# Optimization experiments

Measured on AMD Instinct MI355X. Metric: run time of the kernel, lower is better.

Reference implementation:

```python
import jax, jax.numpy as jnp
import numpy as np

N_NODES = 100000
N_EDGES = 1200000
D = 64
E_CHARGE = np.float32(1.602176634e-19)   # elementary charge (fp32, like the torch buffer)
EPS0 = np.float32(8.8541878128e-12)      # vacuum permittivity (fp32 buffer)


def _mish(x):
    return x * jnp.tanh(jax.nn.softplus(x))


def _mlp(x, w1, b1, w2, b2):
    # nn.Linear convention: y = x @ W.T + b
    h = _mish(x @ w1.T + b1)
    return h @ w2.T + b2


def setup_inputs() -> dict:
    key = jax.random.key(0)
    ks = jax.random.split(key, 20)
    s = 1.0 / np.sqrt(D)
    inp = {
        "node_feats": jax.random.normal(ks[0], (N_NODES, D), jnp.float32),
        "edge_feats": jax.random.normal(ks[1], (N_EDGES, D), jnp.float32),
        "src": jax.random.randint(ks[2], (N_EDGES,), 0, N_NODES),
        "dst": jax.random.randint(ks[3], (N_EDGES,), 0, N_NODES),
    }
    names = ["ws", "wd", "we", "wm"]
    i = 4
    for nm in names:
        inp[nm + "_w1"] = jax.random.normal(ks[i], (D, D), jnp.float32) * s; i += 1
        inp[nm + "_b1"] = jax.random.normal(ks[i], (D,), jnp.float32) * s; i += 1
        inp[nm + "_w2"] = jax.random.normal(ks[i], (D, D), jnp.float32) * s; i += 1
        inp[nm + "_b2"] = jax.random.normal(ks[i], (D,), jnp.float32) * s; i += 1
    return inp


def reference(node_feats, edge_feats, src, dst,
              ws_w1, ws_b1, ws_w2, ws_b2,
              wd_w1, wd_b1, wd_w2, wd_b2,
              we_w1, we_b1, we_w2, we_b2,
              wm_w1, wm_b1, wm_w2, wm_b2):
    # node MLPs then per-edge gather
    h_src = _mlp(node_feats, ws_w1, ws_b1, ws_w2, ws_b2)[src]   # [E, D]
    h_dst = _mlp(node_feats, wd_w1, wd_b1, wd_w2, wd_b2)[dst]   # [E, D]
    ef = _mlp(edge_feats, we_w1, we_b1, we_w2, we_b2)            # [E, D]
    # h_nodes * e^2 / (4*pi*eps0 * edge * 1e-10), all in fp32 like torch
    num = h_src * h_dst * (E_CHARGE ** 2)
    den = np.float32(4.0 * np.pi) * EPS0 * ef * np.float32(1e-10)
    h_nodes = num / den                                          # [E, D]
    m = _mlp(h_nodes, wm_w1, wm_b1, wm_w2, wm_b2)                # [E, D]
    # scatter-sum messages into destination nodes
    h = jax.ops.segment_sum(m, dst, num_segments=N_NODES)        # [N, D]
    return jax.nn.softplus(node_feats + h)
```

## Files before the change

### kernel.cpp

```cpp
#include <hip/hip_runtime.h>
#include <math.h>

#define NNODES 100000
#define NEDGES 1200000
#define TPB_E  5

#define C_EC   1.602176634e-19f
#define C_E2   (C_EC * C_EC)
#define C_4PI  12.566370614359172f
#define C_EPS0 8.8541878128e-12f
#define C_A    (C_4PI * C_EPS0)
#define C_B    1e-10f

typedef __attribute__((ext_vector_type(8))) short bf16x8;
typedef __attribute__((ext_vector_type(4))) float f32x4;
typedef __attribute__((ext_vector_type(4))) unsigned short u16x4;

__device__ __forceinline__ void wave_sync() {
    __builtin_amdgcn_fence(__ATOMIC_ACQ_REL, "wavefront");
    __builtin_amdgcn_wave_barrier();
}

__device__ __forceinline__ unsigned short f2bf(float f) {
    unsigned u = __float_as_uint(f);
    u += 0x7fffu + ((u >> 16) & 1u);
    return (unsigned short)(u >> 16);
}
__device__ __forceinline__ float bf2f(unsigned short s) {
    return __uint_as_float(((unsigned)s) << 16);
}
__device__ __forceinline__ float softplus_f(float x) {
    return fmaxf(x, 0.0f) + log1pf(__expf(-fabsf(x)));
}
__device__ __forceinline__ float mish_f(float x) {
    float e = __expf(fminf(x, 30.0f));
    float n = e * e + 2.0f * e;
    return x * n * __builtin_amdgcn_rcpf(n + 2.0f);
}

__device__ __forceinline__ bf16x8 pack_bf16(float4 a, float4 b) {
    bf16x8 r;
    r[0] = f2bf(a.x); r[1] = f2bf(a.y); r[2] = f2bf(a.z); r[3] = f2bf(a.w);
    r[4] = f2bf(b.x); r[5] = f2bf(b.y); r[6] = f2bf(b.z); r[7] = f2bf(b.w);
    return r;
}


__device__ __forceinline__ void mfma_regs(bf16x8 a0, bf16x8 a1,
                                          const unsigned short* __restrict__ wg,
                                          const float bv[4], int l15, int q,
                                          f32x4 acc[4])
{
    #pragma unroll
    for (int t = 0; t < 4; ++t) {
        acc[t] = (f32x4){bv[t], bv[t], bv[t], bv[t]};
        bf16x8 b0 = *(const bf16x8*)(wg + (t * 16 + l15) * 64 + q * 8);
        bf16x8 b1 = *(const bf16x8*)(wg + (t * 16 + l15) * 64 + 32 + q * 8);
        acc[t] = __builtin_amdgcn_mfma_f32_16x16x32_bf16(a0, b0, acc[t], 0, 0, 0);
        acc[t] = __builtin_amdgcn_mfma_f32_16x16x32_bf16(a1, b1, acc[t], 0, 0, 0);
    }
}

__device__ __forceinline__ void mfma_lds(const unsigned short* hw,
                                         const unsigned short* __restrict__ wg,
                                         const float bv[4], int l15, int q,
                                         f32x4 acc[4])
{
    bf16x8 a0 = *(const bf16x8*)(hw + l15 * 72 + q * 8);
    bf16x8 a1 = *(const bf16x8*)(hw + l15 * 72 + 32 + q * 8);
    mfma_regs(a0, a1, wg, bv, l15, q, acc);
}

__device__ __forceinline__ void mish_to_lds_perm(const f32x4 acc[4], unsigned short* hid, int lane)
{
    const int l15 = lane & 15, q = lane >> 4;
    #pragma unroll
    for (int j = 0; j < 4; ++j) {
        u16x4 v;
        v[0] = f2bf(mish_f(acc[0][j]));
        v[1] = f2bf(mish_f(acc[1][j]));
        v[2] = f2bf(mish_f(acc[2][j]));
        v[3] = f2bf(mish_f(acc[3][j]));
        *(u16x4*)(hid + (q * 4 + j) * 72 + l15 * 4) = v;
    }
}

__global__ __launch_bounds__(256) void convert_w_kernel(
    const float* __restrict__ w0, const float* __restrict__ w1,
    const float* __restrict__ w2, const float* __restrict__ w3,
    const float* __restrict__ w4, const float* __restrict__ w5,
    const float* __restrict__ w6, const float* __restrict__ w7,
    unsigned short* __restrict__ wbf)
{
    int g = blockIdx.x * 256 + threadIdx.x;
    int m = g >> 10;
    int e = (g & 1023) * 4;
    const float* w;
    switch (m) {
        case 0: w = w0; break; case 1: w = w1; break;
        case 2: w = w2; break; case 3: w = w3; break;
        case 4: w = w4; break; case 5: w = w5; break;
        case 6: w = w6; break; default: w = w7; break;
    }
    float4 v = *(const float4*)(w + e);
    int n = e >> 6, k = e & 63;
    bool perm = (m == 1) || (m == 3) || (m >= 5);
    int kk = perm ? ((k & 15) * 4 + (k >> 4)) : k;
    int st = perm ? 4 : 1;
    unsigned short* dp = wbf + m * 4096 + n * 64 + kk;
    dp[0] = f2bf(v.x); dp[st] = f2bf(v.y); dp[2 * st] = f2bf(v.z); dp[3 * st] = f2bf(v.w);
}

__global__ __launch_bounds__(256) void node_mlp_kernel(
    const float* __restrict__ x,
    const unsigned short* __restrict__ wbf,
    const float* __restrict__ bs1, const float* __restrict__ bs2,
    const float* __restrict__ bd1, const float* __restrict__ bd2,
    unsigned short* __restrict__ hs, unsigned short* __restrict__ hd,
    float* __restrict__ out)
{
    __shared__ __align__(16) unsigned short hid[64 * 72];
    const int t = threadIdx.x, lane = t & 63, wave = t >> 6;
    const int row0 = blockIdx.x * 64 + wave * 16;
    unsigned short* hw = hid + wave * 16 * 72;
    const int l15 = lane & 15, q = lane >> 4;

    {
        int r = lane >> 2, c4 = lane & 3;
        if (row0 + r < NNODES) {
            float4 z = make_float4(0.f, 0.f, 0.f, 0.f);
            #pragma unroll
            for (int i = 0; i < 4; ++i)
                *(float4*)(out + (size_t)(row0 + r) * 64 + (c4 + i * 4) * 4) = z;
        }
    }

    float4 v0 = make_float4(0.f,0.f,0.f,0.f), v1 = v0, v2 = v0, v3 = v0;
    {
        int arow = row0 + l15;
        if (arow < NNODES) {
            const float* rp = x + (size_t)arow * 64 + q * 8;
            v0 = *(const float4*)(rp);
            v1 = *(const float4*)(rp + 4);
            v2 = *(const float4*)(rp + 32);
            v3 = *(const float4*)(rp + 36);
        }
    }
    bf16x8 a0 = pack_bf16(v0, v1);
    bf16x8 a1 = pack_bf16(v2, v3);

    float bs1v[4], bs2v[4], bd1v[4], bd2v[4];
    #pragma unroll
    for (int i = 0; i < 4; ++i) {
        bs1v[i] = bs1[i * 16 + l15]; bs2v[i] = bs2[i * 16 + l15];
        bd1v[i] = bd1[i * 16 + l15]; bd2v[i] = bd2[i * 16 + l15];
    }

    f32x4 acc[4];
    mfma_regs(a0, a1, wbf + 0 * 4096, bs1v, l15, q, acc);
    wave_sync();
    mish_to_lds_perm(acc, hw, lane);
    wave_sync();
    mfma_lds(hw, wbf + 1 * 4096, bs2v, l15, q, acc);
    #pragma unroll
    for (int j = 0; j < 4; ++j) {
        int row = row0 + q * 4 + j;
        if (row < NNODES) {
            u16x4 v;
            v[0] = f2bf(acc[0][j]); v[1] = f2bf(acc[1][j]);
            v[2] = f2bf(acc[2][j]); v[3] = f2bf(acc[3][j]);
            *(u16x4*)(hs + (size_t)row * 64 + l15 * 4) = v;
        }
    }
    mfma_regs(a0, a1, wbf + 2 * 4096, bd1v, l15, q, acc);
    wave_sync();
    mish_to_lds_perm(acc, hw, lane);
    wave_sync();
    mfma_lds(hw, wbf + 3 * 4096, bd2v, l15, q, acc);
    #pragma unroll
    for (int j = 0; j < 4; ++j) {
        int row = row0 + q * 4 + j;
        if (row < NNODES) {
            u16x4 v;
            v[0] = f2bf(acc[0][j]); v[1] = f2bf(acc[1][j]);
            v[2] = f2bf(acc[2][j]); v[3] = f2bf(acc[3][j]);
            *(u16x4*)(hd + (size_t)row * 64 + l15 * 4) = v;
        }
    }
}

__device__ __forceinline__ void load_tile(
    int e0, const float* __restrict__ efeat,
    const int* __restrict__ src, const int* __restrict__ dst,
    const unsigned short* __restrict__ hs, const unsigned short* __restrict__ hd,
    int l15, int q,
    float4 v[4], int4& sj, int4& dj, u16x4 va[4], u16x4 vb[4])
{
    const float* rp = efeat + (size_t)(e0 + l15) * 64 + q * 8;
    v[0] = *(const float4*)(rp);
    v[1] = *(const float4*)(rp + 4);
    v[2] = *(const float4*)(rp + 32);
    v[3] = *(const float4*)(rp + 36);
    sj = *(const int4*)(src + e0 + q * 4);
    dj = *(const int4*)(dst + e0 + q * 4);
    const int sjj[4] = {sj.x, sj.y, sj.z, sj.w};
    const int djj[4] = {dj.x, dj.y, dj.z, dj.w};
    #pragma unroll
    for (int j = 0; j < 4; ++j) {
        va[j] = *(const u16x4*)(hs + (size_t)sjj[j] * 64 + l15 * 4);
        vb[j] = *(const u16x4*)(hd + (size_t)djj[j] * 64 + l15 * 4);
    }
}

__global__ __launch_bounds__(256, 4) void edge_kernel(
    const float* __restrict__ efeat,
    const unsigned short* __restrict__ hs, const unsigned short* __restrict__ hd,
    const int* __restrict__ src, const int* __restrict__ dst,
    const unsigned short* __restrict__ wbf,
    const float* __restrict__ be1, const float* __restrict__ be2,
    const float* __restrict__ bm1, const float* __restrict__ bm2,
    float* __restrict__ out)
{
    __shared__ __align__(16) unsigned short hid[64 * 72];
    const int t = threadIdx.x, lane = t & 63, wave = t >> 6;
    unsigned short* hw = hid + wave * 16 * 72;
    const int l15 = lane & 15, q = lane >> 4;
    const int base = blockIdx.x * (4 * TPB_E * 16) + wave * (TPB_E * 16);

    float be1v[4], be2v[4], bm1v[4], bm2v[4];
    #pragma unroll
    for (int i = 0; i < 4; ++i) {
        be1v[i] = be1[i * 16 + l15]; be2v[i] = be2[i * 16 + l15];
        bm1v[i] = bm1[i * 16 + l15]; bm2v[i] = bm2[i * 16 + l15];
    }

    float4 v[4];  int4 sj, dj;  u16x4 va[4], vb[4];
    float4 nv[4]; int4 nsj, ndj; u16x4 nva[4], nvb[4];
    load_tile(base, efeat, src, dst, hs, hd, l15, q, v, sj, dj, va, vb);

    #pragma unroll
    for (int i = 0; i < TPB_E; ++i) {
        bf16x8 a0 = pack_bf16(v[0], v[1]);
        bf16x8 a1 = pack_bf16(v[2], v[3]);
        f32x4 acc[4], ef[4];

        mfma_regs(a0, a1, wbf + 4 * 4096, be1v, l15, q, acc);
        wave_sync();
        mish_to_lds_perm(acc, hw, lane);
        wave_sync();
        mfma_lds(hw, wbf + 5 * 4096, be2v, l15, q, ef);
        wave_sync();

        #pragma unroll
        for (int j = 0; j < 4; ++j) {
            u16x4 hv;
            #pragma unroll
            for (int t4 = 0; t4 < 4; ++t4) {
                float a = bf2f(va[j][t4]);
                float b = bf2f(vb[j][t4]);
                float den = (C_A * ef[t4][j]) * C_B;
                float num = (a * b) * C_E2;
                float h = (den != 0.0f) ? num * __builtin_amdgcn_rcpf(den) : 0.0f;
                h = fminf(fmaxf(h, -1e30f), 1e30f);
                hv[t4] = f2bf(h);
            }
            *(u16x4*)(hw + (q * 4 + j) * 72 + l15 * 4) = hv;
        }
        wave_sync();

        mfma_lds(hw, wbf + 6 * 4096, bm1v, l15, q, acc);
        wave_sync();
        mish_to_lds_perm(acc, hw, lane);
        wave_sync();
        mfma_lds(hw, wbf + 7 * 4096, bm2v, l15, q, acc);

        if (i + 1 < TPB_E)
            load_tile(base + (i + 1) * 16, efeat, src, dst, hs, hd, l15, q,
                      nv, nsj, ndj, nva, nvb);

        const int djj[4] = {dj.x, dj.y, dj.z, dj.w};
        #pragma unroll
        for (int j = 0; j < 4; ++j) {
            float* p = out + (size_t)djj[j] * 64;
            #pragma unroll
            for (int t4 = 0; t4 < 4; ++t4)
                atomicAdd(p + t4 * 16 + l15, acc[t4][j]);
        }

        if (i + 1 < TPB_E) {
            #pragma unroll
            for (int j = 0; j < 4; ++j) { v[j] = nv[j]; va[j] = nva[j]; vb[j] = nvb[j]; }
            sj = nsj; dj = ndj;
        }
    }
}

__global__ __launch_bounds__(256) void finalize_kernel(
    const float* __restrict__ nf, float* __restrict__ out)
{
    int g = blockIdx.x * 256 + threadIdx.x;
    float4 a = ((const float4*)nf)[g];
    float4 h = ((float4*)out)[g];
    float4 o;
    o.x = softplus_f(a.x + h.x);
    o.y = softplus_f(a.y + h.y);
    o.z = softplus_f(a.z + h.z);
    o.w = softplus_f(a.w + h.w);
    ((float4*)out)[g] = o;
}

extern "C" void kernel_launch(void* const* d_in, const int* in_sizes, int n_in,
                              void* d_out, int out_size, void* d_ws, size_t ws_size,
                              hipStream_t stream)
{
    const float* node_feats = (const float*)d_in[0];
    const float* edge_feats = (const float*)d_in[1];
    const int*   src        = (const int*)d_in[2];
    const int*   dst        = (const int*)d_in[3];
    const float* ws_w1 = (const float*)d_in[4];
    const float* ws_b1 = (const float*)d_in[5];
    const float* ws_w2 = (const float*)d_in[6];
    const float* ws_b2 = (const float*)d_in[7];
    const float* wd_w1 = (const float*)d_in[8];
    const float* wd_b1 = (const float*)d_in[9];
    const float* wd_w2 = (const float*)d_in[10];
    const float* wd_b2 = (const float*)d_in[11];
    const float* we_w1 = (const float*)d_in[12];
    const float* we_b1 = (const float*)d_in[13];
    const float* we_w2 = (const float*)d_in[14];
    const float* we_b2 = (const float*)d_in[15];
    const float* wm_w1 = (const float*)d_in[16];
    const float* wm_b1 = (const float*)d_in[17];
    const float* wm_w2 = (const float*)d_in[18];
    const float* wm_b2 = (const float*)d_in[19];

    unsigned short* wbf = (unsigned short*)d_ws;
    unsigned short* hs  = wbf + 8 * 4096;
    unsigned short* hd  = hs + (size_t)NNODES * 64;

    convert_w_kernel<<<32, 256, 0, stream>>>(
        ws_w1, ws_w2, wd_w1, wd_w2, we_w1, we_w2, wm_w1, wm_w2, wbf);

    node_mlp_kernel<<<(NNODES + 63) / 64, 256, 0, stream>>>(
        node_feats, wbf, ws_b1, ws_b2, wd_b1, wd_b2, hs, hd, (float*)d_out);

    edge_kernel<<<NEDGES / (4 * TPB_E * 16), 256, 0, stream>>>(
        edge_feats, hs, hd, src, dst, wbf, we_b1, we_b2, wm_b1, wm_b2, (float*)d_out);

    finalize_kernel<<<(NNODES * 64) / (256 * 4), 256, 0, stream>>>(
        node_feats, (float*)d_out);
}
```

Measured before the change: 920.1 us.

## Process one 16-edge tile per wave and use nontemporal loads for edge streams

The edge kernel drops its per-wave loop over five tiles and the software prefetch of the next tile. Each wave now handles one 16-edge tile and the grid grows to NEDGES/64 blocks, so latency is hidden by having more resident waves instead of explicit double buffering. Edge features and src/dst indices are read with nontemporal loads so streamed data stays out of cache. The launch-bounds occupancy hint is also removed. The trade-off is that bias loads and setup are repeated for every tile, and block scheduling overhead rises.

Result: faster. 794.9 us (-13.6%).

```diff
diff --git a/kernel.cpp b/kernel.cpp
--- a/kernel.cpp
+++ b/kernel.cpp
@@ -3,7 +3,6 @@
 
 #define NNODES 100000
 #define NEDGES 1200000
-#define TPB_E  5
 
 #define C_EC   1.602176634e-19f
 #define C_E2   (C_EC * C_EC)
@@ -14,6 +13,7 @@
 
 typedef __attribute__((ext_vector_type(8))) short bf16x8;
 typedef __attribute__((ext_vector_type(4))) float f32x4;
+typedef __attribute__((ext_vector_type(4))) int   i32x4;
 typedef __attribute__((ext_vector_type(4))) unsigned short u16x4;
 
 __device__ __forceinline__ void wave_sync() {
@@ -38,11 +38,18 @@
     return x * n * __builtin_amdgcn_rcpf(n + 2.0f);
 }
 
-__device__ __forceinline__ bf16x8 pack_bf16(float4 a, float4 b) {
+__device__ __forceinline__ bf16x8 pack_bf16(f32x4 a, f32x4 b) {
     bf16x8 r;
-    r[0] = f2bf(a.x); r[1] = f2bf(a.y); r[2] = f2bf(a.z); r[3] = f2bf(a.w);
-    r[4] = f2bf(b.x); r[5] = f2bf(b.y); r[6] = f2bf(b.z); r[7] = f2bf(b.w);
+    r[0] = f2bf(a[0]); r[1] = f2bf(a[1]); r[2] = f2bf(a[2]); r[3] = f2bf(a[3]);
+    r[4] = f2bf(b[0]); r[5] = f2bf(b[1]); r[6] = f2bf(b[2]); r[7] = f2bf(b[3]);
     return r;
+}
+
+__device__ __forceinline__ f32x4 ldnt4(const float* p) {
+    return __builtin_nontemporal_load((const f32x4*)p);
+}
+__device__ __forceinline__ i32x4 ldnti4(const int* p) {
+    return __builtin_nontemporal_load((const i32x4*)p);
 }
 
 
@@ -135,15 +142,15 @@
         }
     }
 
-    float4 v0 = make_float4(0.f,0.f,0.f,0.f), v1 = v0, v2 = v0, v3 = v0;
+    f32x4 v0 = (f32x4){0.f,0.f,0.f,0.f}, v1 = v0, v2 = v0, v3 = v0;
     {
         int arow = row0 + l15;
         if (arow < NNODES) {
             const float* rp = x + (size_t)arow * 64 + q * 8;
-            v0 = *(const float4*)(rp);
-            v1 = *(const float4*)(rp + 4);
-            v2 = *(const float4*)(rp + 32);
-            v3 = *(const float4*)(rp + 36);
+            v0 = *(const f32x4*)(rp);
+            v1 = *(const f32x4*)(rp + 4);
+            v2 = *(const f32x4*)(rp + 32);
+            v3 = *(const f32x4*)(rp + 36);
         }
     }
     bf16x8 a0 = pack_bf16(v0, v1);
@@ -189,30 +196,7 @@
     }
 }
 
-__device__ __forceinline__ void load_tile(
-    int e0, const float* __restrict__ efeat,
-    const int* __restrict__ src, const int* __restrict__ dst,
-    const unsigned short* __restrict__ hs, const unsigned short* __restrict__ hd,
-    int l15, int q,
-    float4 v[4], int4& sj, int4& dj, u16x4 va[4], u16x4 vb[4])
-{
-    const float* rp = efeat + (size_t)(e0 + l15) * 64 + q * 8;
-    v[0] = *(const float4*)(rp);
-    v[1] = *(const float4*)(rp + 4);
-    v[2] = *(const float4*)(rp + 32);
-    v[3] = *(const float4*)(rp + 36);
-    sj = *(const int4*)(src + e0 + q * 4);
-    dj = *(const int4*)(dst + e0 + q * 4);
-    const int sjj[4] = {sj.x, sj.y, sj.z, sj.w};
-    const int djj[4] = {dj.x, dj.y, dj.z, dj.w};
-    #pragma unroll
-    for (int j = 0; j < 4; ++j) {
-        va[j] = *(const u16x4*)(hs + (size_t)sjj[j] * 64 + l15 * 4);
-        vb[j] = *(const u16x4*)(hd + (size_t)djj[j] * 64 + l15 * 4);
-    }
-}
-
-__global__ __launch_bounds__(256, 4) void edge_kernel(
+__global__ __launch_bounds__(256) void edge_kernel(
     const float* __restrict__ efeat,
     const unsigned short* __restrict__ hs, const unsigned short* __restrict__ hd,
     const int* __restrict__ src, const int* __restrict__ dst,
@@ -223,9 +207,27 @@
 {
     __shared__ __align__(16) unsigned short hid[64 * 72];
     const int t = threadIdx.x, lane = t & 63, wave = t >> 6;
+    const int e0 = blockIdx.x * 64 + wave * 16;
     unsigned short* hw = hid + wave * 16 * 72;
     const int l15 = lane & 15, q = lane >> 4;
-    const int base = blockIdx.x * (4 * TPB_E * 16) + wave * (TPB_E * 16);
+
+    const float* rp = efeat + (size_t)(e0 + l15) * 64 + q * 8;
+    f32x4 v0 = ldnt4(rp);
+    f32x4 v1 = ldnt4(rp + 4);
+    f32x4 v2 = ldnt4(rp + 32);
+    f32x4 v3 = ldnt4(rp + 36);
+
+    i32x4 sj = ldnti4(src + e0 + q * 4);
+    i32x4 dj = ldnti4(dst + e0 + q * 4);
+    const int sjj[4] = {sj[0], sj[1], sj[2], sj[3]};
+    const int djj[4] = {dj[0], dj[1], dj[2], dj[3]};
+
+    u16x4 va[4], vb[4];
+    #pragma unroll
+    for (int j = 0; j < 4; ++j) {
+        va[j] = *(const u16x4*)(hs + (size_t)sjj[j] * 64 + l15 * 4);
+        vb[j] = *(const u16x4*)(hd + (size_t)djj[j] * 64 + l15 * 4);
+    }
 
     float be1v[4], be2v[4], bm1v[4], bm2v[4];
     #pragma unroll
@@ -234,64 +236,46 @@
         bm1v[i] = bm1[i * 16 + l15]; bm2v[i] = bm2[i * 16 + l15];
     }
 
-    float4 v[4];  int4 sj, dj;  u16x4 va[4], vb[4];
-    float4 nv[4]; int4 nsj, ndj; u16x4 nva[4], nvb[4];
-    load_tile(base, efeat, src, dst, hs, hd, l15, q, v, sj, dj, va, vb);
-
-    #pragma unroll
-    for (int i = 0; i < TPB_E; ++i) {
-        bf16x8 a0 = pack_bf16(v[0], v[1]);
-        bf16x8 a1 = pack_bf16(v[2], v[3]);
-        f32x4 acc[4], ef[4];
-
-        mfma_regs(a0, a1, wbf + 4 * 4096, be1v, l15, q, acc);
-        wave_sync();
-        mish_to_lds_perm(acc, hw, lane);
-        wave_sync();
-        mfma_lds(hw, wbf + 5 * 4096, be2v, l15, q, ef);
-        wave_sync();
-
+    bf16x8 a0 = pack_bf16(v0, v1);
+    bf16x8 a1 = pack_bf16(v2, v3);
+    f32x4 acc[4], ef[4];
+
+    mfma_regs(a0, a1, wbf + 4 * 4096, be1v, l15, q, acc);
+    wave_sync();
+    mish_to_lds_perm(acc, hw, lane);
+    wave_sync();
+    mfma_lds(hw, wbf + 5 * 4096, be2v, l15, q, ef);
+    wave_sync();
+
+    #pragma unroll
+    for (int j = 0; j < 4; ++j) {
+        u16x4 hv;
         #pragma unroll
-        for (int j = 0; j < 4; ++j) {
-            u16x4 hv;
-            #pragma unroll
-            for (int t4 = 0; t4 < 4; ++t4) {
-                float a = bf2f(va[j][t4]);
-                float b = bf2f(vb[j][t4]);
-                float den = (C_A * ef[t4][j]) * C_B;
-                float num = (a * b) * C_E2;
-                float h = (den != 0.0f) ? num * __builtin_amdgcn_rcpf(den) : 0.0f;
-                h = fminf(fmaxf(h, -1e30f), 1e30f);
-                hv[t4] = f2bf(h);
-            }
-            *(u16x4*)(hw + (q * 4 + j) * 72 + l15 * 4) = hv;
-        }
-        wave_sync();
-
-        mfma_lds(hw, wbf + 6 * 4096, bm1v, l15, q, acc);
-        wave_sync();
-        mish_to_lds_perm(acc, hw, lane);
-        wave_sync();
-        mfma_lds(hw, wbf + 7 * 4096, bm2v, l15, q, acc);
-
-        if (i + 1 < TPB_E)
-            load_tile(base + (i + 1) * 16, efeat, src, dst, hs, hd, l15, q,
-                      nv, nsj, ndj, nva, nvb);
-
-        const int djj[4] = {dj.x, dj.y, dj.z, dj.w};
+        for (int t4 = 0; t4 < 4; ++t4) {
+            float a = bf2f(va[j][t4]);
+            float b = bf2f(vb[j][t4]);
+            float den = (C_A * ef[t4][j]) * C_B;
+            float num = (a * b) * C_E2;
+            float h = (den != 0.0f) ? num * __builtin_amdgcn_rcpf(den) : 0.0f;
+            h = fminf(fmaxf(h, -1e30f), 1e30f);
+            hv[t4] = f2bf(h);
+        }
+        *(u16x4*)(hw + (q * 4 + j) * 72 + l15 * 4) = hv;
+    }
+    wave_sync();
+
+    mfma_lds(hw, wbf + 6 * 4096, bm1v, l15, q, acc);
+    wave_sync();
+    mish_to_lds_perm(acc, hw, lane);
+    wave_sync();
+    mfma_lds(hw, wbf + 7 * 4096, bm2v, l15, q, acc);
+
+    #pragma unroll
+    for (int j = 0; j < 4; ++j) {
+        float* p = out + (size_t)djj[j] * 64;
         #pragma unroll
-        for (int j = 0; j < 4; ++j) {
-            float* p = out + (size_t)djj[j] * 64;
-            #pragma unroll
-            for (int t4 = 0; t4 < 4; ++t4)
-                atomicAdd(p + t4 * 16 + l15, acc[t4][j]);
-        }
-
-        if (i + 1 < TPB_E) {
-            #pragma unroll
-            for (int j = 0; j < 4; ++j) { v[j] = nv[j]; va[j] = nva[j]; vb[j] = nvb[j]; }
-            sj = nsj; dj = ndj;
-        }
+        for (int t4 = 0; t4 < 4; ++t4)
+            atomicAdd(p + t4 * 16 + l15, acc[t4][j]);
     }
 }
 
@@ -344,7 +328,7 @@
     node_mlp_kernel<<<(NNODES + 63) / 64, 256, 0, stream>>>(
         node_feats, wbf, ws_b1, ws_b2, wd_b1, wd_b2, hs, hd, (float*)d_out);
 
-    edge_kernel<<<NEDGES / (4 * TPB_E * 16), 256, 0, stream>>>(
+    edge_kernel<<<NEDGES / 64, 256, 0, stream>>>(
         edge_feats, hs, hd, src, dst, wbf, we_b1, we_b2, wm_b1, wm_b2, (float*)d_out);
 
     finalize_kernel<<<(NNODES * 64) / (256 * 4), 256, 0, stream>>>(
```
